# Kernel tuning notes

Hardware: AMD Instinct MI355X
Metric: run time of the kernel (lower is better)

Reference implementation:

```python
import jax, jax.numpy as jnp
import numpy as np

N_NODES = 100000
N_EDGES = 1250000
IN_F = 64
HID = 64
N_CLS = 1

def _xavier(key, shape, gain):
    fan_in, fan_out = shape[1], shape[0]
    a = gain * np.sqrt(6.0 / (fan_in + fan_out))
    return jax.random.uniform(key, shape, jnp.float32, -a, a)

def setup_inputs() -> dict:
    key = jax.random.key(0)
    ks = jax.random.split(key, 8)
    x = jax.random.normal(ks[0], (N_NODES, IN_F), jnp.float32)
    e = jax.random.normal(ks[1], (N_EDGES, IN_F), jnp.float32)
    src = jax.random.randint(ks[2], (N_EDGES,), 0, N_NODES, jnp.int64 if jax.config.jax_enable_x64 else jnp.int32)
    dst = jax.random.randint(ks[3], (N_EDGES,), 0, N_NODES, jnp.int64 if jax.config.jax_enable_x64 else jnp.int32)
    W1 = _xavier(ks[4], (IN_F, 3 * IN_F), 0.1)
    b1 = jnp.zeros((IN_F,), jnp.float32)
    W2 = _xavier(ks[5], (HID, IN_F), 0.1)
    b2 = jnp.zeros((HID,), jnp.float32)
    W3 = _xavier(ks[6], (N_CLS, HID), 0.01)
    class_ratio = 0.1
    b3 = jnp.full((N_CLS,), -np.log((1 - class_ratio) / class_ratio), jnp.float32)
    return {"x": x, "e": e, "src": src, "dst": dst,
            "W1": W1, "b1": b1, "W2": W2, "b2": b2, "W3": W3, "b3": b3}

def reference(x, e, src, dst, W1, b1, W2, b2, W3, b3):
    # gather src/dst node features, concat with edge feats: [E, 3*IN_F]
    data = jnp.concatenate((x[src], x[dst], e), axis=1)
    h = jax.nn.relu(data @ W1.T + b1)      # [E, IN_F]  (dropout p=0.0 -> identity)
    h = jax.nn.relu(h @ W2.T + b2)         # [E, HID]
    score = h @ W3.T + b3                  # [E, N_CLS]
    return score
```

## Files before the change

### kernel.cpp

```cpp
#include <hip/hip_runtime.h>

typedef unsigned short u16;
typedef __bf16 bf16;
typedef __bf16 bf16x8 __attribute__((ext_vector_type(8)));
typedef float f32x4 __attribute__((ext_vector_type(4)));

__device__ __forceinline__ float bf2f(u16 u) {
    union { unsigned i; float f; } v; v.i = ((unsigned)u) << 16; return v.f;
}
__device__ __forceinline__ u16 f2bf(float f) {
    unsigned u = __float_as_uint(f);
    return (u16)((u + 0x7FFFu + ((u >> 16) & 1u)) >> 16);
}
__device__ __forceinline__ bf16x8 cvt8(float4 a, float4 b) {
    bf16x8 r;
    r[0] = (bf16)a.x; r[1] = (bf16)a.y; r[2] = (bf16)a.z; r[3] = (bf16)a.w;
    r[4] = (bf16)b.x; r[5] = (bf16)b.y; r[6] = (bf16)b.z; r[7] = (bf16)b.w;
    return r;
}
__device__ __forceinline__ bf16x8 ldg8(const char* rowp, int g, bool bf) {
    if (bf) return ((const bf16x8*)rowp)[g];
    const float4* p = (const float4*)rowp + g * 2;
    return cvt8(p[0], p[1]);
}
__device__ __forceinline__ float ldf(const void* p, int i, bool bf) {
    return bf ? bf2f(((const u16*)p)[i]) : ((const float*)p)[i];
}
__device__ __forceinline__ long getidx(const void* p, long i, bool i64) {
    return i64 ? (long)((const long long*)p)[i] : (long)((const int*)p)[i];
}

__global__ __launch_bounds__(256, 4) void sp_kernel(
    const void* __restrict__ xv,
    const void* __restrict__ ev,
    const void* __restrict__ srcv,
    const void* __restrict__ dstv,
    const void* __restrict__ W1v,
    const void* __restrict__ b1v,
    const void* __restrict__ W2v,
    const void* __restrict__ b2v,
    const void* __restrict__ W3v,
    const void* __restrict__ b3v,
    void* __restrict__ outv,
    int E, long nwt)
{
    const u16 tb3 = *(const u16*)b3v;
    const bool BF = ((tb3 & 0xFF80) == 0xC000);
    const int* s32 = (const int*)srcv;
    const bool I64 = ((s32[1] | s32[3] | s32[5] | s32[7]) == 0);
    const long xrb = BF ? 128 : 256;

    __shared__ __align__(16) char sW1[64 * 384];
    __shared__ __align__(16) char sH1[64 * 128];

    const int tid = threadIdx.x;

    {
        const int row = tid >> 2, q = tid & 3;
        const int rswz = (row & 7) << 4;
        const char* w1r = (const char*)W1v + (long)row * (BF ? 384 : 768);
        #pragma unroll
        for (int i = 0; i < 6; ++i) {
            int g = q + 4 * i;
            bf16x8 v = ldg8(w1r, g, BF);
            *(bf16x8*)(sW1 + row * 384 + ((g * 16) ^ rswz)) = v;
        }
    }
    __syncthreads();

    const int wave = tid >> 6, lane = tid & 63;
    const int lr = lane & 15;
    const int lg = lane >> 4;

    bf16x8 w2f[2][4];
    float bias1[4], bias2[4], w3c[4];
    #pragma unroll
    for (int nt = 0; nt < 4; ++nt) {
        const int c = nt * 16 + lr;
        const char* w2r = (const char*)W2v + (long)c * xrb;
        #pragma unroll
        for (int kt = 0; kt < 2; ++kt)
            w2f[kt][nt] = ldg8(w2r, kt * 4 + lg, BF);
        bias1[nt] = ldf(b1v, c, BF);
        bias2[nt] = ldf(b2v, c, BF);
        w3c[nt]   = ldf(W3v, c, BF);
    }
    const float b3f = ldf(b3v, 0, BF);

    const char* xb = (const char*)xv;
    const char* eb = (const char*)ev;
    const f32x4 z4 = {0.f, 0.f, 0.f, 0.f};

    const long wid = (long)blockIdx.x * 4 + wave;
    const long nw  = (long)gridDim.x * 4;

    long t = wid, s = 0, d = 0;
    if (t < nwt) {
        long ei = t * 16 + lr; if (ei >= E) ei = E - 1;
        s = getidx(srcv, ei, I64);
        d = getidx(dstv, ei, I64);
    }

    for (; t < nwt; t += nw) {
        const long base = t * 16;
        long ei = base + lr; if (ei >= E) ei = E - 1;
        const char* ps = xb + s * xrb;
        const char* pd = xb + d * xrb;
        const char* pe = eb + ei * xrb;

        bf16x8 a[6];
        #pragma unroll
        for (int kt = 0; kt < 2; ++kt) {
            a[kt]     = ldg8(ps, kt * 4 + lg, BF);
            a[2 + kt] = ldg8(pd, kt * 4 + lg, BF);
            a[4 + kt] = ldg8(pe, kt * 4 + lg, BF);
        }

        {
            long tn = t + nw;
            if (tn < nwt) {
                long ein = tn * 16 + lr; if (ein >= E) ein = E - 1;
                s = getidx(srcv, ein, I64);
                d = getidx(dstv, ein, I64);
            }
        }

        f32x4 acc[4] = {z4, z4, z4, z4};
        #pragma unroll
        for (int nt = 0; nt < 4; ++nt) {
            const int wr = nt * 16 + lr, swz = (wr & 7) << 4;
            #pragma unroll
            for (int kt = 0; kt < 6; ++kt) {
                bf16x8 b = *(const bf16x8*)(sW1 + wr * 384 + ((kt * 64 + lg * 16) ^ swz));
                acc[nt] = __builtin_amdgcn_mfma_f32_16x16x32_bf16(a[kt], b, acc[nt], 0, 0, 0);
            }
        }

        #pragma unroll
        for (int nt = 0; nt < 4; ++nt) {
            const int col = nt * 16 + lr;
            const float bias = bias1[nt];
            #pragma unroll
            for (int r = 0; r < 4; ++r) {
                const int hr = wave * 16 + lg * 4 + r;
                float v = acc[nt][r] + bias;
                v = v > 0.f ? v : 0.f;
                *(u16*)(sH1 + hr * 128 + ((col * 2) ^ ((hr & 7) << 4))) = f2bf(v);
            }
        }
        asm volatile("s_waitcnt lgkmcnt(0)" ::: "memory");
        __builtin_amdgcn_sched_barrier(0);

        bf16x8 a2[2];
        {
            const int r = wave * 16 + lr, swz = (r & 7) << 4;
            #pragma unroll
            for (int kt = 0; kt < 2; ++kt)
                a2[kt] = *(const bf16x8*)(sH1 + r * 128 + ((kt * 64 + lg * 16) ^ swz));
        }
        f32x4 acc2[4] = {z4, z4, z4, z4};
        #pragma unroll
        for (int nt = 0; nt < 4; ++nt) {
            #pragma unroll
            for (int kt = 0; kt < 2; ++kt)
                acc2[nt] = __builtin_amdgcn_mfma_f32_16x16x32_bf16(a2[kt], w2f[kt][nt], acc2[nt], 0, 0, 0);
        }

        float sacc[4] = {0.f, 0.f, 0.f, 0.f};
        #pragma unroll
        for (int nt = 0; nt < 4; ++nt) {
            #pragma unroll
            for (int r = 0; r < 4; ++r) {
                float v = acc2[nt][r] + bias2[nt];
                v = v > 0.f ? v : 0.f;
                sacc[r] += v * w3c[nt];
            }
        }
        #pragma unroll
        for (int m = 1; m < 16; m <<= 1) {
            #pragma unroll
            for (int r = 0; r < 4; ++r)
                sacc[r] += __shfl_xor(sacc[r], m, 64);
        }

        if (lr == 0) {
            long e0 = base + lg * 4;
            float v0 = b3f + sacc[0], v1 = b3f + sacc[1];
            float v2 = b3f + sacc[2], v3 = b3f + sacc[3];
            if (e0 + 4 <= E) {
                if (BF) {
                    ushort4 pk = { f2bf(v0), f2bf(v1), f2bf(v2), f2bf(v3) };
                    *(ushort4*)((u16*)outv + e0) = pk;
                } else {
                    float4 pk = { v0, v1, v2, v3 };
                    *(float4*)((float*)outv + e0) = pk;
                }
            } else if (e0 < E) {
                float vv[4] = {v0, v1, v2, v3};
                for (int j = 0; j < 4 && e0 + j < E; ++j) {
                    if (BF) ((u16*)outv)[e0 + j] = f2bf(vv[j]);
                    else    ((float*)outv)[e0 + j] = vv[j];
                }
            }
        }
    }
}

extern "C" void kernel_launch(void* const* d_in, const int* in_sizes, int n_in,
                              void* d_out, int out_size, void* d_ws, size_t ws_size,
                              hipStream_t stream) {
    const int E = in_sizes[2];
    const long nwt = (E + 15) / 16;
    long blocks = (nwt + 3) / 4;
    if (blocks > 1024) blocks = 1024;
    sp_kernel<<<(int)blocks, 256, 0, stream>>>(
        d_in[0], d_in[1], d_in[2], d_in[3], d_in[4], d_in[5],
        d_in[6], d_in[7], d_in[8], d_in[9], d_out, E, nwt);
}
```

Before: 200.3 us.

## Software-pipeline gathered row loads one tile ahead with nontemporal edge loads

Adds register staging so the x[src], x[dst] and edge-feature loads for the next tile are issued before the current tile's MFMA work, and the indices are fetched two tiles ahead. The goal is to hide gather latency behind compute. Edge-feature loads and the output stores become nontemporal to reduce cache pollution, and the W1 shared-memory barrier moves later so the W2 and bias loads overlap with it. The staging buffers raise register pressure, which with launch bounds of 256 threads and 4 blocks could cause spills or lower occupancy.

```diff
diff --git a/kernel.cpp b/kernel.cpp
--- a/kernel.cpp
+++ b/kernel.cpp
@@ -4,6 +4,8 @@
 typedef __bf16 bf16;
 typedef __bf16 bf16x8 __attribute__((ext_vector_type(8)));
 typedef float f32x4 __attribute__((ext_vector_type(4)));
+typedef unsigned int u32x4 __attribute__((ext_vector_type(4)));
+typedef unsigned short u16x4 __attribute__((ext_vector_type(4)));
 
 __device__ __forceinline__ float bf2f(u16 u) {
     union { unsigned i; float f; } v; v.i = ((unsigned)u) << 16; return v.f;
@@ -12,16 +14,29 @@
     unsigned u = __float_as_uint(f);
     return (u16)((u + 0x7FFFu + ((u >> 16) & 1u)) >> 16);
 }
-__device__ __forceinline__ bf16x8 cvt8(float4 a, float4 b) {
+
+struct Gran { u32x4 lo, hi; };
+
+__device__ __forceinline__ Gran ldgran(const char* rowp, int g, bool bf, bool nt) {
+    Gran r;
+    if (bf) {
+        const u32x4* p = (const u32x4*)rowp + g;
+        r.lo = nt ? __builtin_nontemporal_load(p) : *p;
+        r.hi = r.lo;
+    } else {
+        const u32x4* p = (const u32x4*)rowp + g * 2;
+        if (nt) { r.lo = __builtin_nontemporal_load(p); r.hi = __builtin_nontemporal_load(p + 1); }
+        else    { r.lo = p[0]; r.hi = p[1]; }
+    }
+    return r;
+}
+__device__ __forceinline__ bf16x8 tobf(Gran gr, bool bf) {
+    if (bf) { union { u32x4 u; bf16x8 b; } c; c.u = gr.lo; return c.b; }
+    union { u32x4 u; f32x4 f; } a, b; a.u = gr.lo; b.u = gr.hi;
     bf16x8 r;
-    r[0] = (bf16)a.x; r[1] = (bf16)a.y; r[2] = (bf16)a.z; r[3] = (bf16)a.w;
-    r[4] = (bf16)b.x; r[5] = (bf16)b.y; r[6] = (bf16)b.z; r[7] = (bf16)b.w;
+    r[0] = (bf16)a.f[0]; r[1] = (bf16)a.f[1]; r[2] = (bf16)a.f[2]; r[3] = (bf16)a.f[3];
+    r[4] = (bf16)b.f[0]; r[5] = (bf16)b.f[1]; r[6] = (bf16)b.f[2]; r[7] = (bf16)b.f[3];
     return r;
-}
-__device__ __forceinline__ bf16x8 ldg8(const char* rowp, int g, bool bf) {
-    if (bf) return ((const bf16x8*)rowp)[g];
-    const float4* p = (const float4*)rowp + g * 2;
-    return cvt8(p[0], p[1]);
 }
 __device__ __forceinline__ float ldf(const void* p, int i, bool bf) {
     return bf ? bf2f(((const u16*)p)[i]) : ((const float*)p)[i];
@@ -62,11 +77,10 @@
         #pragma unroll
         for (int i = 0; i < 6; ++i) {
             int g = q + 4 * i;
-            bf16x8 v = ldg8(w1r, g, BF);
+            bf16x8 v = tobf(ldgran(w1r, g, BF, false), BF);
             *(bf16x8*)(sW1 + row * 384 + ((g * 16) ^ rswz)) = v;
         }
     }
-    __syncthreads();
 
     const int wave = tid >> 6, lane = tid & 63;
     const int lr = lane & 15;
@@ -80,7 +94,7 @@
         const char* w2r = (const char*)W2v + (long)c * xrb;
         #pragma unroll
         for (int kt = 0; kt < 2; ++kt)
-            w2f[kt][nt] = ldg8(w2r, kt * 4 + lg, BF);
+            w2f[kt][nt] = tobf(ldgran(w2r, kt * 4 + lg, BF, false), BF);
         bias1[nt] = ldf(b1v, c, BF);
         bias2[nt] = ldf(b2v, c, BF);
         w3c[nt]   = ldf(W3v, c, BF);
@@ -94,35 +108,56 @@
     const long wid = (long)blockIdx.x * 4 + wave;
     const long nw  = (long)gridDim.x * 4;
 
-    long t = wid, s = 0, d = 0;
+    __syncthreads();
+
+    Gran stg[6];
+    long s_nx = 0, d_nx = 0;
+    long t = wid;
     if (t < nwt) {
         long ei = t * 16 + lr; if (ei >= E) ei = E - 1;
-        s = getidx(srcv, ei, I64);
-        d = getidx(dstv, ei, I64);
+        long s0 = getidx(srcv, ei, I64);
+        long d0 = getidx(dstv, ei, I64);
+        const char* ps = xb + s0 * xrb;
+        const char* pd = xb + d0 * xrb;
+        const char* pe = eb + ei * xrb;
+        #pragma unroll
+        for (int kt = 0; kt < 2; ++kt) {
+            stg[kt]     = ldgran(ps, kt * 4 + lg, BF, false);
+            stg[2 + kt] = ldgran(pd, kt * 4 + lg, BF, false);
+            stg[4 + kt] = ldgran(pe, kt * 4 + lg, BF, true);
+        }
+        long tn = (t + nw < nwt) ? t + nw : t;
+        long ein = tn * 16 + lr; if (ein >= E) ein = E - 1;
+        s_nx = getidx(srcv, ein, I64);
+        d_nx = getidx(dstv, ein, I64);
     }
 
     for (; t < nwt; t += nw) {
         const long base = t * 16;
-        long ei = base + lr; if (ei >= E) ei = E - 1;
-        const char* ps = xb + s * xrb;
-        const char* pd = xb + d * xrb;
-        const char* pe = eb + ei * xrb;
-
-        bf16x8 a[6];
+        const long tn = t + nw;
+        const bool have_next = tn < nwt;
+
+        long ein = (have_next ? tn : t) * 16 + lr; if (ein >= E) ein = E - 1;
+        const char* psn = xb + s_nx * xrb;
+        const char* pdn = xb + d_nx * xrb;
+        const char* pen = eb + ein * xrb;
+
+        bf16x8 av[6];
+        #pragma unroll
+        for (int j = 0; j < 6; ++j) av[j] = tobf(stg[j], BF);
+
         #pragma unroll
         for (int kt = 0; kt < 2; ++kt) {
-            a[kt]     = ldg8(ps, kt * 4 + lg, BF);
-            a[2 + kt] = ldg8(pd, kt * 4 + lg, BF);
-            a[4 + kt] = ldg8(pe, kt * 4 + lg, BF);
-        }
-
+            stg[kt]     = ldgran(psn, kt * 4 + lg, BF, false);
+            stg[2 + kt] = ldgran(pdn, kt * 4 + lg, BF, false);
+            stg[4 + kt] = ldgran(pen, kt * 4 + lg, BF, true);
+        }
         {
-            long tn = t + nw;
-            if (tn < nwt) {
-                long ein = tn * 16 + lr; if (ein >= E) ein = E - 1;
-                s = getidx(srcv, ein, I64);
-                d = getidx(dstv, ein, I64);
-            }
+            long t2 = t + 2 * nw;
+            long tt = (t2 < nwt) ? t2 : t;
+            long ei2 = tt * 16 + lr; if (ei2 >= E) ei2 = E - 1;
+            s_nx = getidx(srcv, ei2, I64);
+            d_nx = getidx(dstv, ei2, I64);
         }
 
         f32x4 acc[4] = {z4, z4, z4, z4};
@@ -132,7 +167,7 @@
             #pragma unroll
             for (int kt = 0; kt < 6; ++kt) {
                 bf16x8 b = *(const bf16x8*)(sW1 + wr * 384 + ((kt * 64 + lg * 16) ^ swz));
-                acc[nt] = __builtin_amdgcn_mfma_f32_16x16x32_bf16(a[kt], b, acc[nt], 0, 0, 0);
+                acc[nt] = __builtin_amdgcn_mfma_f32_16x16x32_bf16(av[kt], b, acc[nt], 0, 0, 0);
             }
         }
 
@@ -189,11 +224,11 @@
             float v2 = b3f + sacc[2], v3 = b3f + sacc[3];
             if (e0 + 4 <= E) {
                 if (BF) {
-                    ushort4 pk = { f2bf(v0), f2bf(v1), f2bf(v2), f2bf(v3) };
-                    *(ushort4*)((u16*)outv + e0) = pk;
+                    u16x4 pk = { f2bf(v0), f2bf(v1), f2bf(v2), f2bf(v3) };
+                    __builtin_nontemporal_store(pk, (u16x4*)((u16*)outv + e0));
                 } else {
-                    float4 pk = { v0, v1, v2, v3 };
-                    *(float4*)((float*)outv + e0) = pk;
+                    f32x4 pk = { v0, v1, v2, v3 };
+                    __builtin_nontemporal_store(pk, (f32x4*)((float*)outv + e0));
                 }
             } else if (e0 < E) {
                 float vv[4] = {v0, v1, v2, v3};
```

Result: slower. 317.5 us (+58.5%).

## Pre-convert node features to bf16 in workspace before gathered edge MLP

Applied to the files above, without the earlier changes.

Adds a pre-pass kernel that converts the fp32 node feature table to bf16 in the workspace, so the random src/dst gathers in the main kernel read 128-byte rows instead of 256-byte rows. This is meant to cut gather traffic, which dominates with many edges per node. The cost is an extra launch and one streaming pass over the node table. It also moves the shared-memory barrier later so weight loads overlap, and raises the grid cap from 1024 to 1280 blocks.

```diff
diff --git a/kernel.cpp b/kernel.cpp
--- a/kernel.cpp
+++ b/kernel.cpp
@@ -4,6 +4,7 @@
 typedef __bf16 bf16;
 typedef __bf16 bf16x8 __attribute__((ext_vector_type(8)));
 typedef float f32x4 __attribute__((ext_vector_type(4)));
+typedef unsigned int u32x4 __attribute__((ext_vector_type(4)));
 
 __device__ __forceinline__ float bf2f(u16 u) {
     union { unsigned i; float f; } v; v.i = ((unsigned)u) << 16; return v.f;
@@ -12,22 +13,42 @@
     unsigned u = __float_as_uint(f);
     return (u16)((u + 0x7FFFu + ((u >> 16) & 1u)) >> 16);
 }
-__device__ __forceinline__ bf16x8 cvt8(float4 a, float4 b) {
+__device__ __forceinline__ bf16x8 ldg8(const char* rowp, int g, bool bf) {
+    if (bf) {
+        union { u32x4 u; bf16x8 b; } c;
+        c.u = ((const u32x4*)rowp)[g];
+        return c.b;
+    }
+    const f32x4* p = (const f32x4*)rowp + g * 2;
+    f32x4 a = p[0], b = p[1];
     bf16x8 r;
-    r[0] = (bf16)a.x; r[1] = (bf16)a.y; r[2] = (bf16)a.z; r[3] = (bf16)a.w;
-    r[4] = (bf16)b.x; r[5] = (bf16)b.y; r[6] = (bf16)b.z; r[7] = (bf16)b.w;
+    r[0] = (bf16)a[0]; r[1] = (bf16)a[1]; r[2] = (bf16)a[2]; r[3] = (bf16)a[3];
+    r[4] = (bf16)b[0]; r[5] = (bf16)b[1]; r[6] = (bf16)b[2]; r[7] = (bf16)b[3];
     return r;
-}
-__device__ __forceinline__ bf16x8 ldg8(const char* rowp, int g, bool bf) {
-    if (bf) return ((const bf16x8*)rowp)[g];
-    const float4* p = (const float4*)rowp + g * 2;
-    return cvt8(p[0], p[1]);
 }
 __device__ __forceinline__ float ldf(const void* p, int i, bool bf) {
     return bf ? bf2f(((const u16*)p)[i]) : ((const float*)p)[i];
 }
 __device__ __forceinline__ long getidx(const void* p, long i, bool i64) {
     return i64 ? (long)((const long long*)p)[i] : (long)((const int*)p)[i];
+}
+
+__global__ __launch_bounds__(256) void conv_kernel(
+    const void* __restrict__ xv, const void* __restrict__ b3v,
+    u16* __restrict__ xw, long n8)
+{
+    const u16 tb3 = *(const u16*)b3v;
+    if ((tb3 & 0xFF80) == 0xC000) return;
+    const f32x4* src = (const f32x4*)xv;
+    long i = (long)blockIdx.x * blockDim.x + threadIdx.x;
+    const long stride = (long)gridDim.x * blockDim.x;
+    for (; i < n8; i += stride) {
+        f32x4 a = src[i * 2], b = src[i * 2 + 1];
+        union { u32x4 u; bf16x8 v; } c;
+        c.v[0] = (bf16)a[0]; c.v[1] = (bf16)a[1]; c.v[2] = (bf16)a[2]; c.v[3] = (bf16)a[3];
+        c.v[4] = (bf16)b[0]; c.v[5] = (bf16)b[1]; c.v[6] = (bf16)b[2]; c.v[7] = (bf16)b[3];
+        ((u32x4*)xw)[i] = c.u;
+    }
 }
 
 __global__ __launch_bounds__(256, 4) void sp_kernel(
@@ -41,6 +62,8 @@
     const void* __restrict__ b2v,
     const void* __restrict__ W3v,
     const void* __restrict__ b3v,
+    const u16* __restrict__ xw,
+    int use_xw,
     void* __restrict__ outv,
     int E, long nwt)
 {
@@ -50,6 +73,10 @@
     const bool I64 = ((s32[1] | s32[3] | s32[5] | s32[7]) == 0);
     const long xrb = BF ? 128 : 256;
 
+    const bool XBF = BF || (use_xw != 0);
+    const char* xb = (BF || !use_xw) ? (const char*)xv : (const char*)xw;
+    const long xgrb = XBF ? 128 : 256;
+
     __shared__ __align__(16) char sW1[64 * 384];
     __shared__ __align__(16) char sH1[64 * 128];
 
@@ -66,7 +93,6 @@
             *(bf16x8*)(sW1 + row * 384 + ((g * 16) ^ rswz)) = v;
         }
     }
-    __syncthreads();
 
     const int wave = tid >> 6, lane = tid & 63;
     const int lr = lane & 15;
@@ -87,12 +113,13 @@
     }
     const float b3f = ldf(b3v, 0, BF);
 
-    const char* xb = (const char*)xv;
     const char* eb = (const char*)ev;
     const f32x4 z4 = {0.f, 0.f, 0.f, 0.f};
 
     const long wid = (long)blockIdx.x * 4 + wave;
     const long nw  = (long)gridDim.x * 4;
+
+    __syncthreads();
 
     long t = wid, s = 0, d = 0;
     if (t < nwt) {
@@ -104,15 +131,15 @@
     for (; t < nwt; t += nw) {
         const long base = t * 16;
         long ei = base + lr; if (ei >= E) ei = E - 1;
-        const char* ps = xb + s * xrb;
-        const char* pd = xb + d * xrb;
+        const char* ps = xb + s * xgrb;
+        const char* pd = xb + d * xgrb;
         const char* pe = eb + ei * xrb;
 
         bf16x8 a[6];
         #pragma unroll
         for (int kt = 0; kt < 2; ++kt) {
-            a[kt]     = ldg8(ps, kt * 4 + lg, BF);
-            a[2 + kt] = ldg8(pd, kt * 4 + lg, BF);
+            a[kt]     = ldg8(ps, kt * 4 + lg, XBF);
+            a[2 + kt] = ldg8(pd, kt * 4 + lg, XBF);
             a[4 + kt] = ldg8(pe, kt * 4 + lg, BF);
         }
 
@@ -210,10 +237,22 @@
                               void* d_out, int out_size, void* d_ws, size_t ws_size,
                               hipStream_t stream) {
     const int E = in_sizes[2];
+    const long nxe = in_sizes[0];
     const long nwt = (E + 15) / 16;
+
+    const size_t xw_bytes = (size_t)nxe * 2;
+    const int use_xw = (ws_size >= xw_bytes) ? 1 : 0;
+    if (use_xw) {
+        const long n8 = nxe / 8;
+        long cblocks = (n8 + 255) / 256;
+        if (cblocks > 2048) cblocks = 2048;
+        conv_kernel<<<(int)cblocks, 256, 0, stream>>>(d_in[0], d_in[9], (u16*)d_ws, n8);
+    }
+
     long blocks = (nwt + 3) / 4;
-    if (blocks > 1024) blocks = 1024;
+    if (blocks > 1280) blocks = 1280;
     sp_kernel<<<(int)blocks, 256, 0, stream>>>(
         d_in[0], d_in[1], d_in[2], d_in[3], d_in[4], d_in[5],
-        d_in[6], d_in[7], d_in[8], d_in[9], d_out, E, nwt);
-}
+        d_in[6], d_in[7], d_in[8], d_in[9], (const u16*)d_ws, use_xw,
+        d_out, E, nwt);
+}
```

After: 250.4 us. +25.0%, slower.
